# Optimization experiments

Measured on AMD Instinct MI355X. Metric: run time of the kernel, lower is better.

## Reference

```python
import jax, jax.numpy as jnp
import numpy as np

W_PULL = 1.0
W_PUSH = 1.0
W_NORM = 0.001
W_EDGE = 10.0
DELTA_V = 0.5
DELTA_D = 1.5
CE_W = 1.0
DICE_W = 1.0
IGN = -100
NUM_CLASSES = 8
EMBED_DIM = 16
NUM_INST = 16  # instance ids 1..16, 0 = background
EPS_C = 1e-8
EPS_D = 1e-5


def setup_inputs() -> dict:
    key = jax.random.key(0)
    k1, k2, k3, k4 = jax.random.split(key, 4)
    B, D, H, W = 2, 64, 128, 128
    return {
        "sem_logits": jax.random.normal(k1, (B, NUM_CLASSES, D, H, W), jnp.float32),
        "instance_embed": jax.random.normal(k2, (B, EMBED_DIM, D, H, W), jnp.float32),
        "class_labels": jax.random.randint(k3, (B, D, H, W), 0, NUM_CLASSES, dtype=jnp.int32),
        "labels": jax.random.randint(k4, (B, D, H, W), 0, NUM_INST + 1, dtype=jnp.int32),
    }


def _ce_loss(logits, target):
    # nn.CrossEntropyLoss(ignore_index=-100), mean over valid voxels
    logp = jax.nn.log_softmax(logits, axis=1)
    valid = (target != IGN)
    t_safe = jnp.where(valid, target, 0)
    nll = -jnp.take_along_axis(logp, t_safe[:, None].astype(jnp.int32), axis=1)[:, 0]
    v = valid.astype(logits.dtype)
    return (nll * v).sum() / jnp.maximum(v.sum(), 1.0)


def _dice_loss(logits, target):
    C = logits.shape[1]
    probs = jax.nn.softmax(logits, axis=1)
    valid = (target != IGN)
    t_safe = jnp.where(valid, target, 0)
    one_hot = jax.nn.one_hot(t_safe, C, dtype=probs.dtype, axis=1)  # [B,C,D,H,W]
    vm = valid[:, None].astype(probs.dtype)
    probs = probs * vm
    one_hot = one_hot * vm
    axes = tuple(range(2, probs.ndim))
    inter = (probs * one_hot).sum(axes)
    card_p = probs.sum(axes)
    card_g = one_hot.sum(axes)
    dice = (2.0 * inter + EPS_D) / (card_p + card_g + EPS_D)
    return 1.0 - dice.mean()


def _boundary_weight(labels):
    # morphological gradient: 3x3x3 max-pool minus min-pool, replicate pad
    lf = labels.astype(jnp.float32)
    p = jnp.pad(lf, ((0, 0), (1, 1), (1, 1), (1, 1)), mode='edge')
    mx = jax.lax.reduce_window(p, -jnp.inf, jax.lax.max, (1, 3, 3, 3), (1, 1, 1, 1), 'VALID')
    mn = jax.lax.reduce_window(p, jnp.inf, jax.lax.min, (1, 3, 3, 3), (1, 1, 1, 1), 'VALID')
    boundary = (mx != mn).astype(jnp.float32)
    return 1.0 + boundary * (W_EDGE - 1.0)


def _instance_loss(embed, labels, w):
    B, C = embed.shape[:2]
    e_flat = embed.reshape(B, C, -1)   # [B,C,N]
    l_flat = labels.reshape(B, -1)     # [B,N]
    w_flat = w.reshape(B, -1)          # [B,N] (w_bone == 1 since weight_bone==1.0)
    K = NUM_INST

    def per_batch(e, l, wv):
        seg = lambda x: jax.ops.segment_sum(x, l, num_segments=K + 1)
        wsum = seg(wv)                       # [K+1]
        cnt = seg(jnp.ones_like(wv))         # [K+1]
        cnum = seg((e * wv).T)               # [K+1, C]
        centers = cnum / (wsum[:, None] + EPS_C)
        cg = centers[l]                      # [N, C] gather own-instance center
        dist = jnp.linalg.norm(e.T - cg, axis=-1)
        pull_sum = seg(jax.nn.relu(dist - DELTA_V) ** 2 * wv)
        present = cnt[1:] > 0                # ids 1..K
        loss_pull = jnp.where(present, pull_sum[1:] / jnp.maximum(cnt[1:], 1.0), 0.0).sum()
        c = centers[1:]                      # [K, C]
        iu, ju = jnp.triu_indices(K, k=1)
        pw = jnp.linalg.norm(c[iu] - c[ju], axis=-1)
        pv = (present[iu] & present[ju]).astype(pw.dtype)
        npres = present.sum().astype(pw.dtype)
        npairs = npres * (npres - 1.0) / 2.0
        push = jax.nn.relu(2.0 * DELTA_D - pw) ** 2 * pv
        loss_push = jnp.where(npairs > 0, push.sum() / jnp.maximum(npairs, 1.0), 0.0)
        cn = jnp.linalg.norm(c, axis=-1)
        loss_norm = jnp.where(npres > 0, (cn * present).sum() / jnp.maximum(npres, 1.0), 0.0)
        return loss_pull, loss_push, loss_norm, (npres > 0).astype(jnp.float32)

    lp, lpu, ln, val = jax.vmap(per_batch)(e_flat, l_flat, w_flat)
    n = jnp.maximum(val.sum(), 1.0)
    return (W_PULL * lp.sum() + W_PUSH * lpu.sum() + W_NORM * ln.sum()) / n


def reference(sem_logits, instance_embed, class_labels, labels):
    loss_ce = _ce_loss(sem_logits, class_labels)
    loss_dice = _dice_loss(sem_logits, class_labels)
    loss_sem = CE_W * loss_ce + DICE_W * loss_dice
    w_edge = _boundary_weight(labels)
    # weight_bone == 1.0 -> w_bone = ones (scipy EDT branch disabled by module guard)
    loss_ins = _instance_loss(instance_embed, labels, w_edge)
    loss = loss_sem + loss_ins
    return loss, loss_sem, loss_ce, loss_dice, loss_ins
```

## Files before the change

kernel.cpp:

```cpp
#include <hip/hip_runtime.h>

#define DHW (64*128*128)
#define MIR 32

#define OFF_CEM   0
#define OFF_SEGM  1568
#define OFF_PULLM 21152
#define OFF_CTR   22240
#define OFF_CNT   22784
#define ACC_FLOATS 22818
#define OFF_EDGE_BYTES 92160

typedef __bf16 bf16x8 __attribute__((ext_vector_type(8)));
typedef float f32x4 __attribute__((ext_vector_type(4)));
union FragU { short s[8]; bf16x8 v; };

__device__ inline short f2bf(float f) {
    union { float f; unsigned u; } v; v.f = f;
    unsigned r = v.u + 0x7FFF + ((v.u >> 16) & 1);
    return (short)(r >> 16);
}

__device__ inline unsigned edge4(const int* __restrict__ L, int vb, int4 c) {
    int x = vb & 127, y = (vb >> 7) & 127, z = vb >> 14;
    int xm = max(x - 1, 0), xp = min(x + 4, 127);
    unsigned b0 = 0, b1 = 0, b2 = 0, b3 = 0;
#pragma unroll
    for (int dz = -1; dz <= 1; ++dz) {
        int zz = min(max(z + dz, 0), 63);
#pragma unroll
        for (int dy = -1; dy <= 1; ++dy) {
            int yy = min(max(y + dy, 0), 127);
            const int* row = L + (zz << 14) + (yy << 7);
            int4 r = *reinterpret_cast<const int4*>(&row[x]);
            int rm = row[xm], rp = row[xp];
            b0 |= (rm != c.x) | (r.x != c.x) | (r.y != c.x);
            b1 |= (r.x != c.y) | (r.y != c.y) | (r.z != c.y);
            b2 |= (r.y != c.z) | (r.z != c.z) | (r.w != c.z);
            b3 |= (r.z != c.w) | (r.w != c.w) | (rp != c.w);
        }
    }
    return b0 | (b1 << 1) | (b2 << 2) | (b3 << 3);
}

__global__ void zero_kernel(float* acc) {
    int i = blockIdx.x * 1024 + threadIdx.x;
    if (i < ACC_FLOATS) acc[i] = 0.0f;
}

__device__ void ce_role(const float* __restrict__ logits, const int* __restrict__ cls,
                        float* __restrict__ acc, int b, int blk, float* sh) {
    int tid = threadIdx.x;
    int mir = blk & (MIR - 1);
    int vb = (blk * 256 + tid) * 4;
    const float* lg = logits + (size_t)b * 8 * DHW;
    const int* cl = cls + (size_t)b * DHW;

    float4 xc[8];
#pragma unroll
    for (int c = 0; c < 8; ++c)
        xc[c] = *reinterpret_cast<const float4*>(&lg[(size_t)c * DHW + vb]);
    int4 t4 = *reinterpret_cast<const int4*>(&cl[vb]);
    int tt[4] = {t4.x, t4.y, t4.z, t4.w};

    float nll = 0.f, cardp[8], inter[8], cardg[8];
#pragma unroll
    for (int c = 0; c < 8; ++c) { cardp[c] = 0.f; inter[c] = 0.f; cardg[c] = 0.f; }

#pragma unroll
    for (int j = 0; j < 4; ++j) {
        float x[8];
#pragma unroll
        for (int c = 0; c < 8; ++c) x[c] = ((const float*)&xc[c])[j];
        int t = tt[j];
        bool valid = (t != -100);
        float mx = x[0];
#pragma unroll
        for (int c = 1; c < 8; ++c) mx = fmaxf(mx, x[c]);
        float e[8], s = 0.f;
#pragma unroll
        for (int c = 0; c < 8; ++c) { e[c] = __expf(x[c] - mx); s += e[c]; }
        float inv = 1.0f / s;
        float lse = __logf(s);
        if (valid) {
#pragma unroll
            for (int c = 0; c < 8; ++c) {
                float p = e[c] * inv;
                cardp[c] += p;
                if (t == c) { inter[c] += p; cardg[c] += 1.f; nll += mx + lse - x[c]; }
            }
        }
    }

    if (tid < 25) sh[tid] = 0.f;
    __syncthreads();
    int lane = tid & 63;
    float vals[25];
    vals[0] = nll;
#pragma unroll
    for (int c = 0; c < 8; ++c) { vals[1 + c] = cardp[c]; vals[9 + c] = inter[c]; vals[17 + c] = cardg[c]; }
#pragma unroll
    for (int i = 0; i < 25; ++i) {
        float r = vals[i];
#pragma unroll
        for (int off = 32; off > 0; off >>= 1) r += __shfl_down(r, off, 64);
        if (lane == 0) atomicAdd(&sh[i], r);
    }
    __syncthreads();
    if (tid < 25) {
        int dst;
        if (tid == 0) dst = 0;
        else if (tid < 9) dst = 1 + b * 8 + (tid - 1);
        else if (tid < 17) dst = 17 + b * 8 + (tid - 9);
        else dst = 33 + b * 8 + (tid - 17);
        atomicAdd(&acc[OFF_CEM + mir * 49 + dst], sh[tid]);
    }
}

__global__ __launch_bounds__(256) void phaseA_kernel(const float* __restrict__ logits,
                                                     const float* __restrict__ embed,
                                                     const int* __restrict__ cls,
                                                     const int* __restrict__ labels,
                                                     float* __restrict__ acc) {
    __shared__ float smem[352];
    int x = blockIdx.x;
    int g = x / 11, r = x % 11;
    int tid = threadIdx.x;

    if (r >= 8) {
        int ce_idx = g * 3 + (r - 8);
        int b = (ce_idx >= 384) ? 1 : 0;
        int blk = ce_idx - b * 384;
        ce_role(logits, cls, acc, b, blk, smem);
        return;
    }
    int seg_idx = g * 8 + r;
    int b = seg_idx & 1;
    int blk = seg_idx >> 1;
    int mir = blk & (MIR - 1);
    int lane = tid & 63;
    int wv = tid >> 6;
    int m = lane & 15;
    int quad = lane >> 4;

    const int* L = labels + (size_t)b * DHW;
    const float* E = embed + (size_t)b * 16 * DHW + (size_t)m * DHW;

    int waveId = blk * 4 + wv;
    int wavebase = waveId * 256;

    unsigned eb_own;
    {
        int own_off = wavebase + lane * 4;
        int4 lo = *reinterpret_cast<const int4*>(&L[own_off]);
        eb_own = edge4(L, own_off, lo);
    }
    {
        unsigned char* EB = (unsigned char*)acc + OFF_EDGE_BYTES + ((size_t)b << 18);
        EB[blk * 256 + tid] = (unsigned char)eb_own;
    }

    int off = wavebase + quad * 8;

    f32x4 acc_c = {0.f, 0.f, 0.f, 0.f};
    f32x4 acc_w = {0.f, 0.f, 0.f, 0.f};
    f32x4 acc_n = {0.f, 0.f, 0.f, 0.f};

    FragU ones_col;
#pragma unroll
    for (int j = 0; j < 8; ++j) ones_col.s[j] = (m == 0) ? (short)0x3F80 : (short)0;

    int4 La0 = *reinterpret_cast<const int4*>(&L[off]);
    int4 La1 = *reinterpret_cast<const int4*>(&L[off + 4]);
    float4 Fa0 = *reinterpret_cast<const float4*>(&E[off]);
    float4 Fa1 = *reinterpret_cast<const float4*>(&E[off + 4]);
    int4 Lb0 = *reinterpret_cast<const int4*>(&L[off + 32]);
    int4 Lb1 = *reinterpret_cast<const int4*>(&L[off + 36]);
    float4 Fb0 = *reinterpret_cast<const float4*>(&E[off + 32]);
    float4 Fb1 = *reinterpret_cast<const float4*>(&E[off + 36]);

#pragma unroll
    for (int i = 0; i < 8; ++i) {
        int4 cl0, cl1; float4 cf0, cf1;
        if (i & 1) { cl0 = Lb0; cl1 = Lb1; cf0 = Fb0; cf1 = Fb1; }
        else       { cl0 = La0; cl1 = La1; cf0 = Fa0; cf1 = Fa1; }
        if (i < 6) {
            int noff = off + (i + 2) * 32;
            if (i & 1) {
                Lb0 = *reinterpret_cast<const int4*>(&L[noff]);
                Lb1 = *reinterpret_cast<const int4*>(&L[noff + 4]);
                Fb0 = *reinterpret_cast<const float4*>(&E[noff]);
                Fb1 = *reinterpret_cast<const float4*>(&E[noff + 4]);
            } else {
                La0 = *reinterpret_cast<const int4*>(&L[noff]);
                La1 = *reinterpret_cast<const int4*>(&L[noff + 4]);
                Fa0 = *reinterpret_cast<const float4*>(&E[noff]);
                Fa1 = *reinterpret_cast<const float4*>(&E[noff + 4]);
            }
        }
        int s0 = i * 8 + quad * 2;
        unsigned ebA = (unsigned)__shfl((int)eb_own, s0, 64);
        unsigned ebB = (unsigned)__shfl((int)eb_own, s0 + 1, 64);
        unsigned eb = (ebA & 0xF) | ((ebB & 0xF) << 4);

        int ls[8] = {cl0.x, cl0.y, cl0.z, cl0.w, cl1.x, cl1.y, cl1.z, cl1.w};
        float fs[8] = {cf0.x, cf0.y, cf0.z, cf0.w, cf1.x, cf1.y, cf1.z, cf1.w};

        FragU a, a2, bf;
#pragma unroll
        for (int j = 0; j < 8; ++j) {
            short w = ((eb >> j) & 1) ? (short)0x4120 : (short)0x3F80;
            bool hit = (ls[j] == m + 1);
            a.s[j]  = hit ? w : (short)0;
            a2.s[j] = hit ? (short)0x3F80 : (short)0;
            bf.s[j] = f2bf(fs[j]);
        }
        acc_c = __builtin_amdgcn_mfma_f32_16x16x32_bf16(a.v, bf.v, acc_c, 0, 0, 0);
        acc_w = __builtin_amdgcn_mfma_f32_16x16x32_bf16(a.v, ones_col.v, acc_w, 0, 0, 0);
        acc_n = __builtin_amdgcn_mfma_f32_16x16x32_bf16(a2.v, ones_col.v, acc_n, 0, 0, 0);
    }

    float* cacc = smem;
    for (int i = tid; i < 288; i += 256) cacc[i] = 0.f;
    __syncthreads();
#pragma unroll
    for (int rr = 0; rr < 4; ++rr)
        atomicAdd(&cacc[(quad * 4 + rr) * 16 + m], acc_c[rr]);
    if (m == 0) {
#pragma unroll
        for (int rr = 0; rr < 4; ++rr) {
            atomicAdd(&cacc[256 + quad * 4 + rr], acc_w[rr]);
            atomicAdd(&cacc[272 + quad * 4 + rr], acc_n[rr]);
        }
    }
    __syncthreads();
    {
        float* segbase = acc + OFF_SEGM + mir * 612 + b * 306;
        atomicAdd(&segbase[16 + tid], cacc[tid]);
        if (tid < 16) atomicAdd(&segbase[272 + 1 + tid], cacc[256 + tid]);
        else if (tid < 32) atomicAdd(&segbase[289 + 1 + (tid - 16)], cacc[256 + tid]);
    }
}

__global__ __launch_bounds__(1024) void centers_kernel(float* acc) {
    int tid = threadIdx.x;
    if (tid < 544) {
        int b = tid / 272, r = tid % 272;
        int k = r >> 4;
        float cn = 0.f, ws = 0.f;
        for (int mv = 0; mv < MIR; ++mv) {
            const float* segbase = acc + OFF_SEGM + mv * 612 + b * 306;
            if (r >= 16) cn += segbase[r];
            ws += segbase[272 + k];
        }
        acc[OFF_CTR + tid] = (r >= 16) ? cn / (ws + 1e-8f) : 0.f;
    } else if (tid < 578) {
        int j = tid - 544;
        int b = j / 17, k = j % 17;
        float s = 0.f;
        for (int mv = 0; mv < MIR; ++mv)
            s += acc[OFF_SEGM + mv * 612 + b * 306 + 289 + k];
        acc[OFF_CNT + j] = s;
    }
}

__global__ __launch_bounds__(256) void phaseB_kernel(const float* __restrict__ logits,
                                                     const float* __restrict__ embed,
                                                     const int* __restrict__ cls,
                                                     const int* __restrict__ labels,
                                                     float* __restrict__ acc) {
    __shared__ float smem[352];
    int x = blockIdx.x;
    int g = x / 13, r = x % 13;
    int tid = threadIdx.x;

    if (r >= 8) {
        int ce_idx = g * 5 + (r - 8);
        int b = (ce_idx >= 640) ? 1 : 0;
        int blk = 384 + (ce_idx - b * 640);
        ce_role(logits, cls, acc, b, blk, smem);
        return;
    }
    int pull_idx = g * 8 + r;
    int b = pull_idx & 1;
    int blk = pull_idx >> 1;
    int wv = tid >> 6;
    float* ctr = smem;
    float* ps = smem + 272;
    for (int i = tid; i < 272; i += 256) ctr[i] = acc[OFF_CTR + b * 272 + i];
    for (int i = tid; i < 80; i += 256) ps[i] = 0.f;
    __syncthreads();

    const int* L = labels + (size_t)b * DHW;
    const float* E = embed + (size_t)b * 16 * DHW;
    int vb = (blk * 256 + tid) * 4;

    int4 l4 = *reinterpret_cast<const int4*>(&L[vb]);
    int l[4] = {l4.x, l4.y, l4.z, l4.w};
    unsigned eb;
    {
        const unsigned char* EB = (const unsigned char*)acc + OFF_EDGE_BYTES + ((size_t)b << 18);
        eb = EB[blk * 256 + tid];
    }

    float d2a[4] = {0.f, 0.f, 0.f, 0.f};
#pragma unroll
    for (int q = 0; q < 4; ++q) {
        float4 e0 = *reinterpret_cast<const float4*>(&E[(size_t)(4 * q + 0) * DHW + vb]);
        float4 e1 = *reinterpret_cast<const float4*>(&E[(size_t)(4 * q + 1) * DHW + vb]);
        float4 e2 = *reinterpret_cast<const float4*>(&E[(size_t)(4 * q + 2) * DHW + vb]);
        float4 e3 = *reinterpret_cast<const float4*>(&E[(size_t)(4 * q + 3) * DHW + vb]);
#pragma unroll
        for (int j = 0; j < 4; ++j) {
            if (l[j] != 0) {
                float4 cv = *reinterpret_cast<const float4*>(&ctr[l[j] * 16 + q * 4]);
                float d0 = ((const float*)&e0)[j] - cv.x;
                float d1 = ((const float*)&e1)[j] - cv.y;
                float d2 = ((const float*)&e2)[j] - cv.z;
                float d3 = ((const float*)&e3)[j] - cv.w;
                d2a[j] += d0 * d0 + d1 * d1 + d2 * d2 + d3 * d3;
            }
        }
    }

#pragma unroll
    for (int j = 0; j < 4; ++j) {
        if (l[j] != 0) {
            float w = ((eb >> j) & 1) ? 10.f : 1.f;
            float d = fmaxf(sqrtf(d2a[j]) - 0.5f, 0.f);
            atomicAdd(&ps[wv * 20 + l[j]], d * d * w);
        }
    }
    __syncthreads();
    if (tid >= 1 && tid < 17) {
        float v = ps[tid] + ps[20 + tid] + ps[40 + tid] + ps[60 + tid];
        int mir = blk & (MIR - 1);
        if (v != 0.f) atomicAdd(&acc[OFF_PULLM + mir * 34 + b * 17 + tid], v);
    }
}

__global__ __launch_bounds__(256) void finalize_kernel(const float* __restrict__ acc, float* __restrict__ out) {
    __shared__ float s_ce[49], s_pl[34];
    __shared__ float sh_push[2], sh_norm[2], sh_pull[2], sh_npres[2];
    int tid = threadIdx.x;
    if (tid < 49) {
        float s = 0.f;
        for (int mv = 0; mv < MIR; ++mv) s += acc[OFF_CEM + mv * 49 + tid];
        s_ce[tid] = s;
    }
    if (tid >= 64 && tid < 98) {
        int j = tid - 64;
        float s = 0.f;
        for (int mv = 0; mv < MIR; ++mv) s += acc[OFF_PULLM + mv * 34 + j];
        s_pl[j] = s;
    }
    if (tid < 2) { sh_push[tid] = 0.f; sh_norm[tid] = 0.f; sh_pull[tid] = 0.f; sh_npres[tid] = 0.f; }
    __syncthreads();

    if (tid < 32) {
        int b = tid >> 4, k = (tid & 15) + 1;
        float cnt = acc[OFF_CNT + b * 17 + k];
        if (cnt > 0.f) {
            atomicAdd(&sh_npres[b], 1.f);
            atomicAdd(&sh_pull[b], s_pl[b * 17 + k] / fmaxf(cnt, 1.f));
            const float* c = &acc[OFF_CTR + (b * 17 + k) * 16];
            float n2 = 0.f;
            for (int i = 0; i < 16; ++i) n2 += c[i] * c[i];
            atomicAdd(&sh_norm[b], sqrtf(n2));
        }
    }
    for (int t = tid; t < 240; t += blockDim.x) {
        int b = t / 120, p = t % 120;
        int i = 1, rem = p;
        while (rem >= (16 - i)) { rem -= (16 - i); ++i; }
        int j = i + 1 + rem;
        bool pi = acc[OFF_CNT + b * 17 + i] > 0.f;
        bool pj = acc[OFF_CNT + b * 17 + j] > 0.f;
        if (pi && pj) {
            const float* ci = &acc[OFF_CTR + (b * 17 + i) * 16];
            const float* cj = &acc[OFF_CTR + (b * 17 + j) * 16];
            float d2 = 0.f;
            for (int c = 0; c < 16; ++c) { float dd = ci[c] - cj[c]; d2 += dd * dd; }
            float r = fmaxf(3.0f - sqrtf(d2), 0.f);
            atomicAdd(&sh_push[b], r * r);
        }
    }
    __syncthreads();
    if (tid == 0) {
        float nll = s_ce[0];
        float vcnt = 0.f;
        for (int i = 0; i < 16; ++i) vcnt += s_ce[33 + i];
        float ce = nll / fmaxf(vcnt, 1.f);
        float dsum = 0.f;
        for (int i = 0; i < 16; ++i) {
            float it = s_ce[17 + i], cp = s_ce[1 + i], cg = s_ce[33 + i];
            dsum += (2.f * it + 1e-5f) / (cp + cg + 1e-5f);
        }
        float dice = 1.f - dsum / 16.f;
        float lp = 0.f, lpu = 0.f, ln = 0.f, val = 0.f;
        for (int b = 0; b < 2; ++b) {
            float npres = sh_npres[b];
            lp += sh_pull[b];
            float npairs = npres * (npres - 1.f) * 0.5f;
            lpu += (npairs > 0.f) ? sh_push[b] / fmaxf(npairs, 1.f) : 0.f;
            ln += (npres > 0.f) ? sh_norm[b] / fmaxf(npres, 1.f) : 0.f;
            val += (npres > 0.f) ? 1.f : 0.f;
        }
        float n = fmaxf(val, 1.f);
        float ins = (1.0f * lp + 1.0f * lpu + 0.001f * ln) / n;
        float sem = ce + dice;
        out[0] = sem + ins;
        out[1] = sem;
        out[2] = ce;
        out[3] = dice;
        out[4] = ins;
    }
}

extern "C" void kernel_launch(void* const* d_in, const int* in_sizes, int n_in,
                              void* d_out, int out_size, void* d_ws, size_t ws_size,
                              hipStream_t stream) {
    const float* sem = (const float*)d_in[0];
    const float* emb = (const float*)d_in[1];
    const int* cls = (const int*)d_in[2];
    const int* lab = (const int*)d_in[3];
    float* out = (float*)d_out;
    float* acc = (float*)d_ws;

    hipLaunchKernelGGL(zero_kernel, dim3(23), dim3(1024), 0, stream, acc);
    hipLaunchKernelGGL(phaseA_kernel, dim3(2816), dim3(256), 0, stream, sem, emb, cls, lab, acc);
    hipLaunchKernelGGL(centers_kernel, dim3(1), dim3(1024), 0, stream, acc);
    hipLaunchKernelGGL(phaseB_kernel, dim3(3328), dim3(256), 0, stream, sem, emb, cls, lab, acc);
    hipLaunchKernelGGL(finalize_kernel, dim3(1), dim3(256), 0, stream, acc, out);
}
```

Measured before the change: 307.5 us.

## Fuse five launches into one cooperative persistent kernel with grid syncs

Replaces the zero, phaseA, centers, phaseB and finalize launches with one cooperative kernel that loops over tasks and separates phases with grid.sync(). Centers are now computed redundantly in every block directly into shared memory instead of by a separate single-block kernel. CE/dice work is regrouped into per-batch half-size tasks, run after the seg or pull tasks instead of interleaved with them. The aim is to remove launch gaps and the serial single-block stages, at the cost of grid-barrier overhead, less overlap between CE and embedding work, and a fallback to the old path if the cooperative launch fails.

```diff
diff --git a/kernel.cpp b/kernel.cpp
--- a/kernel.cpp
+++ b/kernel.cpp
@@ -1,4 +1,7 @@
 #include <hip/hip_runtime.h>
+#include <hip/hip_cooperative_groups.h>
+
+namespace cg = cooperative_groups;
 
 #define DHW (64*128*128)
 #define MIR 32
@@ -43,100 +46,12 @@
     return b0 | (b1 << 1) | (b2 << 2) | (b3 << 3);
 }
 
-__global__ void zero_kernel(float* acc) {
-    int i = blockIdx.x * 1024 + threadIdx.x;
-    if (i < ACC_FLOATS) acc[i] = 0.0f;
-}
-
-__device__ void ce_role(const float* __restrict__ logits, const int* __restrict__ cls,
-                        float* __restrict__ acc, int b, int blk, float* sh) {
-    int tid = threadIdx.x;
-    int mir = blk & (MIR - 1);
-    int vb = (blk * 256 + tid) * 4;
-    const float* lg = logits + (size_t)b * 8 * DHW;
-    const int* cl = cls + (size_t)b * DHW;
-
-    float4 xc[8];
-#pragma unroll
-    for (int c = 0; c < 8; ++c)
-        xc[c] = *reinterpret_cast<const float4*>(&lg[(size_t)c * DHW + vb]);
-    int4 t4 = *reinterpret_cast<const int4*>(&cl[vb]);
-    int tt[4] = {t4.x, t4.y, t4.z, t4.w};
-
-    float nll = 0.f, cardp[8], inter[8], cardg[8];
-#pragma unroll
-    for (int c = 0; c < 8; ++c) { cardp[c] = 0.f; inter[c] = 0.f; cardg[c] = 0.f; }
-
-#pragma unroll
-    for (int j = 0; j < 4; ++j) {
-        float x[8];
-#pragma unroll
-        for (int c = 0; c < 8; ++c) x[c] = ((const float*)&xc[c])[j];
-        int t = tt[j];
-        bool valid = (t != -100);
-        float mx = x[0];
-#pragma unroll
-        for (int c = 1; c < 8; ++c) mx = fmaxf(mx, x[c]);
-        float e[8], s = 0.f;
-#pragma unroll
-        for (int c = 0; c < 8; ++c) { e[c] = __expf(x[c] - mx); s += e[c]; }
-        float inv = 1.0f / s;
-        float lse = __logf(s);
-        if (valid) {
-#pragma unroll
-            for (int c = 0; c < 8; ++c) {
-                float p = e[c] * inv;
-                cardp[c] += p;
-                if (t == c) { inter[c] += p; cardg[c] += 1.f; nll += mx + lse - x[c]; }
-            }
-        }
-    }
-
-    if (tid < 25) sh[tid] = 0.f;
-    __syncthreads();
-    int lane = tid & 63;
-    float vals[25];
-    vals[0] = nll;
-#pragma unroll
-    for (int c = 0; c < 8; ++c) { vals[1 + c] = cardp[c]; vals[9 + c] = inter[c]; vals[17 + c] = cardg[c]; }
-#pragma unroll
-    for (int i = 0; i < 25; ++i) {
-        float r = vals[i];
-#pragma unroll
-        for (int off = 32; off > 0; off >>= 1) r += __shfl_down(r, off, 64);
-        if (lane == 0) atomicAdd(&sh[i], r);
-    }
-    __syncthreads();
-    if (tid < 25) {
-        int dst;
-        if (tid == 0) dst = 0;
-        else if (tid < 9) dst = 1 + b * 8 + (tid - 1);
-        else if (tid < 17) dst = 17 + b * 8 + (tid - 9);
-        else dst = 33 + b * 8 + (tid - 17);
-        atomicAdd(&acc[OFF_CEM + mir * 49 + dst], sh[tid]);
-    }
-}
-
-__global__ __launch_bounds__(256) void phaseA_kernel(const float* __restrict__ logits,
-                                                     const float* __restrict__ embed,
-                                                     const int* __restrict__ cls,
-                                                     const int* __restrict__ labels,
-                                                     float* __restrict__ acc) {
-    __shared__ float smem[352];
-    int x = blockIdx.x;
-    int g = x / 11, r = x % 11;
-    int tid = threadIdx.x;
-
-    if (r >= 8) {
-        int ce_idx = g * 3 + (r - 8);
-        int b = (ce_idx >= 384) ? 1 : 0;
-        int blk = ce_idx - b * 384;
-        ce_role(logits, cls, acc, b, blk, smem);
-        return;
-    }
-    int seg_idx = g * 8 + r;
-    int b = seg_idx & 1;
-    int blk = seg_idx >> 1;
+
+__device__ void seg_task(const float* __restrict__ embed, const int* __restrict__ labels,
+                         float* __restrict__ acc, int t, float* cacc) {
+    int tid = threadIdx.x;
+    int b = t & 1;
+    int blk = t >> 1;
     int mir = blk & (MIR - 1);
     int lane = tid & 63;
     int wv = tid >> 6;
@@ -220,7 +135,6 @@
         acc_n = __builtin_amdgcn_mfma_f32_16x16x32_bf16(a2.v, ones_col.v, acc_n, 0, 0, 0);
     }
 
-    float* cacc = smem;
     for (int i = tid; i < 288; i += 256) cacc[i] = 0.f;
     __syncthreads();
 #pragma unroll
@@ -240,54 +154,85 @@
         if (tid < 16) atomicAdd(&segbase[272 + 1 + tid], cacc[256 + tid]);
         else if (tid < 32) atomicAdd(&segbase[289 + 1 + (tid - 16)], cacc[256 + tid]);
     }
-}
-
-__global__ __launch_bounds__(1024) void centers_kernel(float* acc) {
-    int tid = threadIdx.x;
-    if (tid < 544) {
-        int b = tid / 272, r = tid % 272;
-        int k = r >> 4;
-        float cn = 0.f, ws = 0.f;
-        for (int mv = 0; mv < MIR; ++mv) {
-            const float* segbase = acc + OFF_SEGM + mv * 612 + b * 306;
-            if (r >= 16) cn += segbase[r];
-            ws += segbase[272 + k];
-        }
-        acc[OFF_CTR + tid] = (r >= 16) ? cn / (ws + 1e-8f) : 0.f;
-    } else if (tid < 578) {
-        int j = tid - 544;
-        int b = j / 17, k = j % 17;
-        float s = 0.f;
-        for (int mv = 0; mv < MIR; ++mv)
-            s += acc[OFF_SEGM + mv * 612 + b * 306 + 289 + k];
-        acc[OFF_CNT + j] = s;
-    }
-}
-
-__global__ __launch_bounds__(256) void phaseB_kernel(const float* __restrict__ logits,
-                                                     const float* __restrict__ embed,
-                                                     const int* __restrict__ cls,
-                                                     const int* __restrict__ labels,
-                                                     float* __restrict__ acc) {
-    __shared__ float smem[352];
-    int x = blockIdx.x;
-    int g = x / 13, r = x % 13;
-    int tid = threadIdx.x;
-
-    if (r >= 8) {
-        int ce_idx = g * 5 + (r - 8);
-        int b = (ce_idx >= 640) ? 1 : 0;
-        int blk = 384 + (ce_idx - b * 640);
-        ce_role(logits, cls, acc, b, blk, smem);
-        return;
-    }
-    int pull_idx = g * 8 + r;
-    int b = pull_idx & 1;
-    int blk = pull_idx >> 1;
+    __syncthreads();
+}
+
+__device__ void ce_half(const float* __restrict__ logits, const int* __restrict__ cls,
+                        float* __restrict__ acc, int b, int h, float* sh) {
+    int tid = threadIdx.x;
+    int mir = h & (MIR - 1);
+    int vb = h * 512 + tid * 2;
+    const float* lg = logits + (size_t)b * 8 * DHW;
+    const int* cl = cls + (size_t)b * DHW;
+
+    float2 xc[8];
+#pragma unroll
+    for (int c = 0; c < 8; ++c)
+        xc[c] = *reinterpret_cast<const float2*>(&lg[(size_t)c * DHW + vb]);
+    int2 t2 = *reinterpret_cast<const int2*>(&cl[vb]);
+    int tt[2] = {t2.x, t2.y};
+
+    float nll = 0.f, cardp[8], inter[8], cardg[8];
+#pragma unroll
+    for (int c = 0; c < 8; ++c) { cardp[c] = 0.f; inter[c] = 0.f; cardg[c] = 0.f; }
+
+#pragma unroll
+    for (int j = 0; j < 2; ++j) {
+        float x[8];
+#pragma unroll
+        for (int c = 0; c < 8; ++c) x[c] = j ? xc[c].y : xc[c].x;
+        int tgt = tt[j];
+        bool valid = (tgt != -100);
+        float mx = x[0];
+#pragma unroll
+        for (int c = 1; c < 8; ++c) mx = fmaxf(mx, x[c]);
+        float e[8], s = 0.f;
+#pragma unroll
+        for (int c = 0; c < 8; ++c) { e[c] = __expf(x[c] - mx); s += e[c]; }
+        float inv = 1.0f / s;
+        float lse = __logf(s);
+        if (valid) {
+#pragma unroll
+            for (int c = 0; c < 8; ++c) {
+                float p = e[c] * inv;
+                cardp[c] += p;
+                if (tgt == c) { inter[c] += p; cardg[c] += 1.f; nll += mx + lse - x[c]; }
+            }
+        }
+    }
+
+    if (tid < 25) sh[tid] = 0.f;
+    __syncthreads();
+    int lane = tid & 63;
+    float vals[25];
+    vals[0] = nll;
+#pragma unroll
+    for (int c = 0; c < 8; ++c) { vals[1 + c] = cardp[c]; vals[9 + c] = inter[c]; vals[17 + c] = cardg[c]; }
+#pragma unroll
+    for (int i = 0; i < 25; ++i) {
+        float r = vals[i];
+#pragma unroll
+        for (int off = 32; off > 0; off >>= 1) r += __shfl_down(r, off, 64);
+        if (lane == 0) atomicAdd(&sh[i], r);
+    }
+    __syncthreads();
+    if (tid < 25) {
+        int dst;
+        if (tid == 0) dst = 0;
+        else if (tid < 9) dst = 1 + b * 8 + (tid - 1);
+        else if (tid < 17) dst = 17 + b * 8 + (tid - 9);
+        else dst = 33 + b * 8 + (tid - 17);
+        atomicAdd(&acc[OFF_CEM + mir * 49 + dst], sh[tid]);
+    }
+    __syncthreads();
+}
+
+__device__ void pull_task(const float* __restrict__ embed, const int* __restrict__ labels,
+                          float* __restrict__ acc, int t, const float* __restrict__ ctr, float* ps) {
+    int tid = threadIdx.x;
+    int b = t & 1;
+    int blk = t >> 1;
     int wv = tid >> 6;
-    float* ctr = smem;
-    float* ps = smem + 272;
-    for (int i = tid; i < 272; i += 256) ctr[i] = acc[OFF_CTR + b * 272 + i];
     for (int i = tid; i < 80; i += 256) ps[i] = 0.f;
     __syncthreads();
 
@@ -337,9 +282,10 @@
         int mir = blk & (MIR - 1);
         if (v != 0.f) atomicAdd(&acc[OFF_PULLM + mir * 34 + b * 17 + tid], v);
     }
-}
-
-__global__ __launch_bounds__(256) void finalize_kernel(const float* __restrict__ acc, float* __restrict__ out) {
+    __syncthreads();
+}
+
+__device__ void finalize_dev(const float* __restrict__ acc, float* __restrict__ out) {
     __shared__ float s_ce[49], s_pl[34];
     __shared__ float sh_push[2], sh_norm[2], sh_pull[2], sh_npres[2];
     int tid = threadIdx.x;
@@ -417,6 +363,190 @@
     }
 }
 
+__global__ __launch_bounds__(256) void fused_kernel(const float* __restrict__ logits,
+                                                    const float* __restrict__ embed,
+                                                    const int* __restrict__ cls,
+                                                    const int* __restrict__ labels,
+                                                    float* __restrict__ acc,
+                                                    float* __restrict__ out) {
+    cg::grid_group grid = cg::this_grid();
+    __shared__ float smem[400];
+    int tid = threadIdx.x;
+    int nb = gridDim.x;
+
+    for (int i = blockIdx.x * 256 + tid; i < ACC_FLOATS; i += nb * 256) acc[i] = 0.f;
+    grid.sync();
+
+    for (int t = blockIdx.x; t < 2048; t += nb) seg_task(embed, labels, acc, t, smem);
+    for (int t = blockIdx.x; t < 2048; t += nb) ce_half(logits, cls, acc, 0, t, smem + 352);
+    grid.sync();
+
+    {
+        int b = blockIdx.x & 1;
+        int k = 1 + (tid >> 4), c = tid & 15;
+        float cn = 0.f, ws = 0.f;
+        for (int mv = 0; mv < MIR; ++mv) {
+            const float* segbase = acc + OFF_SEGM + mv * 612 + b * 306;
+            cn += segbase[k * 16 + c];
+            ws += segbase[272 + k];
+        }
+        float cv = cn / (ws + 1e-8f);
+        smem[k * 16 + c] = cv;
+        if (tid < 16) smem[tid] = 0.f;
+        if (blockIdx.x < 2) {
+            acc[OFF_CTR + b * 272 + k * 16 + c] = cv;
+            if (tid < 17) {
+                float s = 0.f;
+                for (int mv = 0; mv < MIR; ++mv)
+                    s += acc[OFF_SEGM + mv * 612 + b * 306 + 289 + tid];
+                acc[OFF_CNT + b * 17 + tid] = s;
+            }
+        }
+        __syncthreads();
+    }
+    for (int t = blockIdx.x; t < 2048; t += nb) pull_task(embed, labels, acc, t, smem, smem + 288);
+    for (int t = blockIdx.x; t < 2048; t += nb) ce_half(logits, cls, acc, 1, t, smem + 352);
+    grid.sync();
+
+    if (blockIdx.x == 0) finalize_dev(acc, out);
+}
+
+__global__ void zero_kernel(float* acc) {
+    int i = blockIdx.x * 1024 + threadIdx.x;
+    if (i < ACC_FLOATS) acc[i] = 0.0f;
+}
+
+__device__ void ce_role4(const float* __restrict__ logits, const int* __restrict__ cls,
+                         float* __restrict__ acc, int b, int blk, float* sh) {
+    int tid = threadIdx.x;
+    int mir = blk & (MIR - 1);
+    int vb = (blk * 256 + tid) * 4;
+    const float* lg = logits + (size_t)b * 8 * DHW;
+    const int* cl = cls + (size_t)b * DHW;
+    float4 xc[8];
+#pragma unroll
+    for (int c = 0; c < 8; ++c)
+        xc[c] = *reinterpret_cast<const float4*>(&lg[(size_t)c * DHW + vb]);
+    int4 t4 = *reinterpret_cast<const int4*>(&cl[vb]);
+    int tt[4] = {t4.x, t4.y, t4.z, t4.w};
+    float nll = 0.f, cardp[8], inter[8], cardg[8];
+#pragma unroll
+    for (int c = 0; c < 8; ++c) { cardp[c] = 0.f; inter[c] = 0.f; cardg[c] = 0.f; }
+#pragma unroll
+    for (int j = 0; j < 4; ++j) {
+        float x[8];
+#pragma unroll
+        for (int c = 0; c < 8; ++c) x[c] = ((const float*)&xc[c])[j];
+        int t = tt[j];
+        bool valid = (t != -100);
+        float mx = x[0];
+#pragma unroll
+        for (int c = 1; c < 8; ++c) mx = fmaxf(mx, x[c]);
+        float e[8], s = 0.f;
+#pragma unroll
+        for (int c = 0; c < 8; ++c) { e[c] = __expf(x[c] - mx); s += e[c]; }
+        float inv = 1.0f / s;
+        float lse = __logf(s);
+        if (valid) {
+#pragma unroll
+            for (int c = 0; c < 8; ++c) {
+                float p = e[c] * inv;
+                cardp[c] += p;
+                if (t == c) { inter[c] += p; cardg[c] += 1.f; nll += mx + lse - x[c]; }
+            }
+        }
+    }
+    if (tid < 25) sh[tid] = 0.f;
+    __syncthreads();
+    int lane = tid & 63;
+    float vals[25];
+    vals[0] = nll;
+#pragma unroll
+    for (int c = 0; c < 8; ++c) { vals[1 + c] = cardp[c]; vals[9 + c] = inter[c]; vals[17 + c] = cardg[c]; }
+#pragma unroll
+    for (int i = 0; i < 25; ++i) {
+        float r = vals[i];
+#pragma unroll
+        for (int off = 32; off > 0; off >>= 1) r += __shfl_down(r, off, 64);
+        if (lane == 0) atomicAdd(&sh[i], r);
+    }
+    __syncthreads();
+    if (tid < 25) {
+        int dst;
+        if (tid == 0) dst = 0;
+        else if (tid < 9) dst = 1 + b * 8 + (tid - 1);
+        else if (tid < 17) dst = 17 + b * 8 + (tid - 9);
+        else dst = 33 + b * 8 + (tid - 17);
+        atomicAdd(&acc[OFF_CEM + mir * 49 + dst], sh[tid]);
+    }
+}
+
+__global__ __launch_bounds__(256) void phaseA_kernel(const float* __restrict__ logits,
+                                                     const float* __restrict__ embed,
+                                                     const int* __restrict__ cls,
+                                                     const int* __restrict__ labels,
+                                                     float* __restrict__ acc) {
+    __shared__ float smem[352];
+    int x = blockIdx.x;
+    int g = x / 11, r = x % 11;
+    if (r >= 8) {
+        int ce_idx = g * 3 + (r - 8);
+        int b = (ce_idx >= 384) ? 1 : 0;
+        ce_role4(logits, cls, acc, b, ce_idx - b * 384, smem);
+        return;
+    }
+    seg_task(embed, labels, acc, g * 8 + r, smem);
+}
+
+__global__ __launch_bounds__(1024) void centers_kernel(float* acc) {
+    int tid = threadIdx.x;
+    if (tid < 544) {
+        int b = tid / 272, r = tid % 272;
+        int k = r >> 4;
+        float cn = 0.f, ws = 0.f;
+        for (int mv = 0; mv < MIR; ++mv) {
+            const float* segbase = acc + OFF_SEGM + mv * 612 + b * 306;
+            if (r >= 16) cn += segbase[r];
+            ws += segbase[272 + k];
+        }
+        acc[OFF_CTR + tid] = (r >= 16) ? cn / (ws + 1e-8f) : 0.f;
+    } else if (tid < 578) {
+        int j = tid - 544;
+        int b = j / 17, k = j % 17;
+        float s = 0.f;
+        for (int mv = 0; mv < MIR; ++mv)
+            s += acc[OFF_SEGM + mv * 612 + b * 306 + 289 + k];
+        acc[OFF_CNT + j] = s;
+    }
+}
+
+__global__ __launch_bounds__(256) void phaseB_kernel(const float* __restrict__ logits,
+                                                     const float* __restrict__ embed,
+                                                     const int* __restrict__ cls,
+                                                     const int* __restrict__ labels,
+                                                     float* __restrict__ acc) {
+    __shared__ float smem[352];
+    int x = blockIdx.x;
+    int g = x / 13, r = x % 13;
+    int tid = threadIdx.x;
+    if (r >= 8) {
+        int ce_idx = g * 5 + (r - 8);
+        int b = (ce_idx >= 640) ? 1 : 0;
+        ce_role4(logits, cls, acc, b, 384 + (ce_idx - b * 640), smem);
+        return;
+    }
+    int t = g * 8 + r;
+    int b = t & 1;
+    float* ctr = smem;
+    for (int i = tid; i < 272; i += 256) ctr[i] = acc[OFF_CTR + b * 272 + i];
+    __syncthreads();
+    pull_task(embed, labels, acc, t, ctr, smem + 288);
+}
+
+__global__ __launch_bounds__(256) void finalize_kernel(const float* __restrict__ acc, float* __restrict__ out) {
+    finalize_dev(acc, out);
+}
+
 extern "C" void kernel_launch(void* const* d_in, const int* in_sizes, int n_in,
                               void* d_out, int out_size, void* d_ws, size_t ws_size,
                               hipStream_t stream) {
@@ -427,9 +557,33 @@
     float* out = (float*)d_out;
     float* acc = (float*)d_ws;
 
-    hipLaunchKernelGGL(zero_kernel, dim3(23), dim3(1024), 0, stream, acc);
-    hipLaunchKernelGGL(phaseA_kernel, dim3(2816), dim3(256), 0, stream, sem, emb, cls, lab, acc);
-    hipLaunchKernelGGL(centers_kernel, dim3(1), dim3(1024), 0, stream, acc);
-    hipLaunchKernelGGL(phaseB_kernel, dim3(3328), dim3(256), 0, stream, sem, emb, cls, lab, acc);
-    hipLaunchKernelGGL(finalize_kernel, dim3(1), dim3(256), 0, stream, acc, out);
-}
+    static int g_grid = -1;
+    if (g_grid < 0) {
+        int nb = 0;
+        if (hipOccupancyMaxActiveBlocksPerMultiprocessor(&nb, fused_kernel, 256, 0) == hipSuccess && nb >= 1) {
+            hipDeviceProp_t prop;
+            int dev = 0;
+            hipGetDevice(&dev);
+            if (hipGetDeviceProperties(&prop, dev) == hipSuccess) {
+                long cap = (long)nb * prop.multiProcessorCount;
+                int g = 2048;
+                while (g > 256 && g > cap) g >>= 1;
+                g_grid = (cap >= 256) ? g : 0;
+            } else g_grid = 0;
+        } else g_grid = 0;
+    }
+
+    bool done = false;
+    if (g_grid > 0) {
+        void* args[] = {(void*)&sem, (void*)&emb, (void*)&cls, (void*)&lab, (void*)&acc, (void*)&out};
+        if (hipLaunchCooperativeKernel(fused_kernel, dim3(g_grid), dim3(256), args, 0, stream) == hipSuccess)
+            done = true;
+    }
+    if (!done) {
+        hipLaunchKernelGGL(zero_kernel, dim3(23), dim3(1024), 0, stream, acc);
+        hipLaunchKernelGGL(phaseA_kernel, dim3(2816), dim3(256), 0, stream, sem, emb, cls, lab, acc);
+        hipLaunchKernelGGL(centers_kernel, dim3(1), dim3(1024), 0, stream, acc);
+        hipLaunchKernelGGL(phaseB_kernel, dim3(3328), dim3(256), 0, stream, sem, emb, cls, lab, acc);
+        hipLaunchKernelGGL(finalize_kernel, dim3(1), dim3(256), 0, stream, acc, out);
+    }
+}
```

Result: slower. 530.7 us (+72.6%).

## Stage label halo tile in LDS for boundary stencil and MFMA label reads

Applied to the files above, without the earlier changes.

Phase A now cooperatively loads a 3x10-row label halo tile into shared memory. The 27-point boundary stencil is evaluated from that tile, and the MFMA loop reads its labels from the tile and its edge bits from a shared byte array instead of global loads and wave shuffles. Phase B hoists all 16 embedding-channel loads ahead of the distance loop so more memory requests are in flight. This cuts redundant global and L2 label traffic, at the cost of about 16 KB of LDS per block, which may lower occupancy, plus extra barriers and higher register pressure in phase B.

```diff
diff --git a/kernel.cpp b/kernel.cpp
--- a/kernel.cpp
+++ b/kernel.cpp
@@ -21,28 +21,6 @@
     return (short)(r >> 16);
 }
 
-__device__ inline unsigned edge4(const int* __restrict__ L, int vb, int4 c) {
-    int x = vb & 127, y = (vb >> 7) & 127, z = vb >> 14;
-    int xm = max(x - 1, 0), xp = min(x + 4, 127);
-    unsigned b0 = 0, b1 = 0, b2 = 0, b3 = 0;
-#pragma unroll
-    for (int dz = -1; dz <= 1; ++dz) {
-        int zz = min(max(z + dz, 0), 63);
-#pragma unroll
-        for (int dy = -1; dy <= 1; ++dy) {
-            int yy = min(max(y + dy, 0), 127);
-            const int* row = L + (zz << 14) + (yy << 7);
-            int4 r = *reinterpret_cast<const int4*>(&row[x]);
-            int rm = row[xm], rp = row[xp];
-            b0 |= (rm != c.x) | (r.x != c.x) | (r.y != c.x);
-            b1 |= (r.x != c.y) | (r.y != c.y) | (r.z != c.y);
-            b2 |= (r.y != c.z) | (r.z != c.z) | (r.w != c.z);
-            b3 |= (r.z != c.w) | (r.w != c.w) | (rp != c.w);
-        }
-    }
-    return b0 | (b1 << 1) | (b2 << 2) | (b3 << 3);
-}
-
 __global__ void zero_kernel(float* acc) {
     int i = blockIdx.x * 1024 + threadIdx.x;
     if (i < ACC_FLOATS) acc[i] = 0.0f;
@@ -122,19 +100,21 @@
                                                      const int* __restrict__ cls,
                                                      const int* __restrict__ labels,
                                                      float* __restrict__ acc) {
-    __shared__ float smem[352];
+    __shared__ int s_tile[3840];
+    __shared__ unsigned char s_eb[256];
+    __shared__ float s_cacc[288];
     int x = blockIdx.x;
-    int g = x / 11, r = x % 11;
+    int g = x / 11, r3 = x % 11;
     int tid = threadIdx.x;
 
-    if (r >= 8) {
-        int ce_idx = g * 3 + (r - 8);
+    if (r3 >= 8) {
+        int ce_idx = g * 3 + (r3 - 8);
         int b = (ce_idx >= 384) ? 1 : 0;
         int blk = ce_idx - b * 384;
-        ce_role(logits, cls, acc, b, blk, smem);
+        ce_role(logits, cls, acc, b, blk, s_cacc);
         return;
     }
-    int seg_idx = g * 8 + r;
+    int seg_idx = g * 8 + r3;
     int b = seg_idx & 1;
     int blk = seg_idx >> 1;
     int mir = blk & (MIR - 1);
@@ -146,21 +126,48 @@
     const int* L = labels + (size_t)b * DHW;
     const float* E = embed + (size_t)b * 16 * DHW + (size_t)m * DHW;
 
-    int waveId = blk * 4 + wv;
-    int wavebase = waveId * 256;
-
-    unsigned eb_own;
+    int vb0 = blk * 1024;
+    int z0 = vb0 >> 14;
+    int y0 = (vb0 >> 7) & 127;
+
+    for (int idx = tid; idx < 960; idx += 256) {
+        int row = idx >> 5, col = idx & 31;
+        int zi = row / 10, ri = row - zi * 10;
+        int zz = min(max(z0 + zi - 1, 0), 63);
+        int yy = min(max(y0 + ri - 1, 0), 127);
+        reinterpret_cast<int4*>(s_tile)[row * 32 + col] =
+            *reinterpret_cast<const int4*>(&L[(zz << 14) + (yy << 7) + col * 4]);
+    }
+    __syncthreads();
+
     {
-        int own_off = wavebase + lane * 4;
-        int4 lo = *reinterpret_cast<const int4*>(&L[own_off]);
-        eb_own = edge4(L, own_off, lo);
-    }
-    {
+        int p = tid * 4;
+        int xx = p & 127, lr = p >> 7;
+        int xm = max(xx - 1, 0), xp = min(xx + 4, 127);
+        const int* crow = &s_tile[(10 + lr + 1) * 128];
+        int4 c; c.x = crow[xx]; c.y = crow[xx + 1]; c.z = crow[xx + 2]; c.w = crow[xx + 3];
+        unsigned b0 = 0, b1 = 0, b2 = 0, b3 = 0;
+#pragma unroll
+        for (int zi = 0; zi < 3; ++zi) {
+#pragma unroll
+            for (int dy = 0; dy < 3; ++dy) {
+                const int* row = &s_tile[(zi * 10 + lr + dy) * 128];
+                int rx = row[xx], ry = row[xx + 1], rz = row[xx + 2], rw = row[xx + 3];
+                int rm = row[xm], rp = row[xp];
+                b0 |= (rm != c.x) | (rx != c.x) | (ry != c.x);
+                b1 |= (rx != c.y) | (ry != c.y) | (rz != c.y);
+                b2 |= (ry != c.z) | (rz != c.z) | (rw != c.z);
+                b3 |= (rz != c.w) | (rw != c.w) | (rp != c.w);
+            }
+        }
+        unsigned eb_own = b0 | (b1 << 1) | (b2 << 2) | (b3 << 3);
+        s_eb[tid] = (unsigned char)eb_own;
         unsigned char* EB = (unsigned char*)acc + OFF_EDGE_BYTES + ((size_t)b << 18);
         EB[blk * 256 + tid] = (unsigned char)eb_own;
     }
-
-    int off = wavebase + quad * 8;
+    __syncthreads();
+
+    int lo0 = wv * 256 + quad * 8;
 
     f32x4 acc_c = {0.f, 0.f, 0.f, 0.f};
     f32x4 acc_w = {0.f, 0.f, 0.f, 0.f};
@@ -170,75 +177,66 @@
 #pragma unroll
     for (int j = 0; j < 8; ++j) ones_col.s[j] = (m == 0) ? (short)0x3F80 : (short)0;
 
-    int4 La0 = *reinterpret_cast<const int4*>(&L[off]);
-    int4 La1 = *reinterpret_cast<const int4*>(&L[off + 4]);
-    float4 Fa0 = *reinterpret_cast<const float4*>(&E[off]);
-    float4 Fa1 = *reinterpret_cast<const float4*>(&E[off + 4]);
-    int4 Lb0 = *reinterpret_cast<const int4*>(&L[off + 32]);
-    int4 Lb1 = *reinterpret_cast<const int4*>(&L[off + 36]);
-    float4 Fb0 = *reinterpret_cast<const float4*>(&E[off + 32]);
-    float4 Fb1 = *reinterpret_cast<const float4*>(&E[off + 36]);
+    int goff = vb0 + lo0;
+    float4 Fa0 = *reinterpret_cast<const float4*>(&E[goff]);
+    float4 Fa1 = *reinterpret_cast<const float4*>(&E[goff + 4]);
+    float4 Fb0 = *reinterpret_cast<const float4*>(&E[goff + 32]);
+    float4 Fb1 = *reinterpret_cast<const float4*>(&E[goff + 36]);
 
 #pragma unroll
     for (int i = 0; i < 8; ++i) {
-        int4 cl0, cl1; float4 cf0, cf1;
-        if (i & 1) { cl0 = Lb0; cl1 = Lb1; cf0 = Fb0; cf1 = Fb1; }
-        else       { cl0 = La0; cl1 = La1; cf0 = Fa0; cf1 = Fa1; }
+        float4 cf0, cf1;
+        if (i & 1) { cf0 = Fb0; cf1 = Fb1; }
+        else       { cf0 = Fa0; cf1 = Fa1; }
         if (i < 6) {
-            int noff = off + (i + 2) * 32;
+            int noff = goff + (i + 2) * 32;
             if (i & 1) {
-                Lb0 = *reinterpret_cast<const int4*>(&L[noff]);
-                Lb1 = *reinterpret_cast<const int4*>(&L[noff + 4]);
                 Fb0 = *reinterpret_cast<const float4*>(&E[noff]);
                 Fb1 = *reinterpret_cast<const float4*>(&E[noff + 4]);
             } else {
-                La0 = *reinterpret_cast<const int4*>(&L[noff]);
-                La1 = *reinterpret_cast<const int4*>(&L[noff + 4]);
                 Fa0 = *reinterpret_cast<const float4*>(&E[noff]);
                 Fa1 = *reinterpret_cast<const float4*>(&E[noff + 4]);
             }
         }
+        int lo = lo0 + i * 32;
+        const int* rowp = &s_tile[(10 + (lo >> 7) + 1) * 128 + (lo & 127)];
         int s0 = i * 8 + quad * 2;
-        unsigned ebA = (unsigned)__shfl((int)eb_own, s0, 64);
-        unsigned ebB = (unsigned)__shfl((int)eb_own, s0 + 1, 64);
-        unsigned eb = (ebA & 0xF) | ((ebB & 0xF) << 4);
-
-        int ls[8] = {cl0.x, cl0.y, cl0.z, cl0.w, cl1.x, cl1.y, cl1.z, cl1.w};
-        float fs[8] = {cf0.x, cf0.y, cf0.z, cf0.w, cf1.x, cf1.y, cf1.z, cf1.w};
+        unsigned short u = *reinterpret_cast<const unsigned short*>(&s_eb[wv * 64 + s0]);
+        unsigned eb = (u & 0xF) | ((u >> 4) & 0xF0);
 
         FragU a, a2, bf;
 #pragma unroll
         for (int j = 0; j < 8; ++j) {
             short w = ((eb >> j) & 1) ? (short)0x4120 : (short)0x3F80;
-            bool hit = (ls[j] == m + 1);
+            bool hit = (rowp[j] == m + 1);
             a.s[j]  = hit ? w : (short)0;
             a2.s[j] = hit ? (short)0x3F80 : (short)0;
-            bf.s[j] = f2bf(fs[j]);
+            float fv = (j < 4) ? ((const float*)&cf0)[j] : ((const float*)&cf1)[j - 4];
+            bf.s[j] = f2bf(fv);
         }
         acc_c = __builtin_amdgcn_mfma_f32_16x16x32_bf16(a.v, bf.v, acc_c, 0, 0, 0);
         acc_w = __builtin_amdgcn_mfma_f32_16x16x32_bf16(a.v, ones_col.v, acc_w, 0, 0, 0);
         acc_n = __builtin_amdgcn_mfma_f32_16x16x32_bf16(a2.v, ones_col.v, acc_n, 0, 0, 0);
     }
 
-    float* cacc = smem;
-    for (int i = tid; i < 288; i += 256) cacc[i] = 0.f;
+    for (int i = tid; i < 288; i += 256) s_cacc[i] = 0.f;
     __syncthreads();
 #pragma unroll
     for (int rr = 0; rr < 4; ++rr)
-        atomicAdd(&cacc[(quad * 4 + rr) * 16 + m], acc_c[rr]);
+        atomicAdd(&s_cacc[(quad * 4 + rr) * 16 + m], acc_c[rr]);
     if (m == 0) {
 #pragma unroll
         for (int rr = 0; rr < 4; ++rr) {
-            atomicAdd(&cacc[256 + quad * 4 + rr], acc_w[rr]);
-            atomicAdd(&cacc[272 + quad * 4 + rr], acc_n[rr]);
+            atomicAdd(&s_cacc[256 + quad * 4 + rr], acc_w[rr]);
+            atomicAdd(&s_cacc[272 + quad * 4 + rr], acc_n[rr]);
         }
     }
     __syncthreads();
     {
         float* segbase = acc + OFF_SEGM + mir * 612 + b * 306;
-        atomicAdd(&segbase[16 + tid], cacc[tid]);
-        if (tid < 16) atomicAdd(&segbase[272 + 1 + tid], cacc[256 + tid]);
-        else if (tid < 32) atomicAdd(&segbase[289 + 1 + (tid - 16)], cacc[256 + tid]);
+        atomicAdd(&segbase[16 + tid], s_cacc[tid]);
+        if (tid < 16) atomicAdd(&segbase[272 + 1 + tid], s_cacc[256 + tid]);
+        else if (tid < 32) atomicAdd(&segbase[289 + 1 + (tid - 16)], s_cacc[256 + tid]);
     }
 }
 
@@ -271,17 +269,17 @@
                                                      float* __restrict__ acc) {
     __shared__ float smem[352];
     int x = blockIdx.x;
-    int g = x / 13, r = x % 13;
+    int g = x / 13, r3 = x % 13;
     int tid = threadIdx.x;
 
-    if (r >= 8) {
-        int ce_idx = g * 5 + (r - 8);
+    if (r3 >= 8) {
+        int ce_idx = g * 5 + (r3 - 8);
         int b = (ce_idx >= 640) ? 1 : 0;
         int blk = 384 + (ce_idx - b * 640);
         ce_role(logits, cls, acc, b, blk, smem);
         return;
     }
-    int pull_idx = g * 8 + r;
+    int pull_idx = g * 8 + r3;
     int b = pull_idx & 1;
     int blk = pull_idx >> 1;
     int wv = tid >> 6;
@@ -303,21 +301,22 @@
         eb = EB[blk * 256 + tid];
     }
 
+    float4 ev[16];
+#pragma unroll
+    for (int c = 0; c < 16; ++c)
+        ev[c] = *reinterpret_cast<const float4*>(&E[(size_t)c * DHW + vb]);
+
     float d2a[4] = {0.f, 0.f, 0.f, 0.f};
 #pragma unroll
     for (int q = 0; q < 4; ++q) {
-        float4 e0 = *reinterpret_cast<const float4*>(&E[(size_t)(4 * q + 0) * DHW + vb]);
-        float4 e1 = *reinterpret_cast<const float4*>(&E[(size_t)(4 * q + 1) * DHW + vb]);
-        float4 e2 = *reinterpret_cast<const float4*>(&E[(size_t)(4 * q + 2) * DHW + vb]);
-        float4 e3 = *reinterpret_cast<const float4*>(&E[(size_t)(4 * q + 3) * DHW + vb]);
 #pragma unroll
         for (int j = 0; j < 4; ++j) {
             if (l[j] != 0) {
                 float4 cv = *reinterpret_cast<const float4*>(&ctr[l[j] * 16 + q * 4]);
-                float d0 = ((const float*)&e0)[j] - cv.x;
-                float d1 = ((const float*)&e1)[j] - cv.y;
-                float d2 = ((const float*)&e2)[j] - cv.z;
-                float d3 = ((const float*)&e3)[j] - cv.w;
+                float d0 = ((const float*)&ev[4 * q + 0])[j] - cv.x;
+                float d1 = ((const float*)&ev[4 * q + 1])[j] - cv.y;
+                float d2 = ((const float*)&ev[4 * q + 2])[j] - cv.z;
+                float d3 = ((const float*)&ev[4 * q + 3])[j] - cv.w;
                 d2a[j] += d0 * d0 + d1 * d1 + d2 * d2 + d3 * d3;
             }
         }
```

New measurement: 306.6 us. No clear change (-0.3%).
